# Kernel optimization log

Measured on AMD Instinct MI355X. Metric: run time of the kernel, lower is better.

The kernel has to match this reference:

```python
import jax, jax.numpy as jnp
import numpy as np

D_MODEL = 1024
NUM_HEADS = 16
D_HEAD = D_MODEL // NUM_HEADS
MAX_SEQ_LEN = 2048
THETA = 10000.0
BATCH = 2
SEQ = 2048


def _rope_tables():
    # inv_freq over even dims; emb interleaves each freq twice: [f0,f0,f1,f1,...]
    inv_freq = 1.0 / (THETA ** (jnp.arange(0, D_HEAD, 2, dtype=jnp.float32) / D_HEAD))
    t = jnp.arange(MAX_SEQ_LEN, dtype=jnp.float32)
    freqs = jnp.einsum('i,j->ij', t, inv_freq)  # [S, d_head/2]
    emb = jnp.stack((freqs, freqs), axis=-1).reshape(MAX_SEQ_LEN, D_HEAD)
    return jnp.cos(emb), jnp.sin(emb)


def _rotate_half(x):
    # pairwise interleaved rotation: (x0,x1,x2,x3,...) -> (-x1,x0,-x3,x2,...)
    xr = x.reshape(x.shape[:-1] + (D_HEAD // 2, 2))
    x1, x2 = xr[..., 0], xr[..., 1]
    return jnp.stack((-x2, x1), axis=-1).reshape(x.shape)


def setup_inputs() -> dict:
    key = jax.random.key(0)
    ks = jax.random.split(key, 5)
    std = np.sqrt(2.0 / (D_MODEL + D_MODEL)).astype(np.float32)
    return {
        'in_features': jax.random.normal(ks[0], (BATCH, SEQ, D_MODEL), dtype=jnp.float32),
        'token_positions': jnp.arange(SEQ, dtype=jnp.int64) if jax.config.jax_enable_x64 else jnp.arange(SEQ, dtype=jnp.int32),
        'wq': jax.random.normal(ks[1], (D_MODEL, D_MODEL), dtype=jnp.float32) * std,
        'wk': jax.random.normal(ks[2], (D_MODEL, D_MODEL), dtype=jnp.float32) * std,
        'wv': jax.random.normal(ks[3], (D_MODEL, D_MODEL), dtype=jnp.float32) * std,
        'wo': jax.random.normal(ks[4], (D_MODEL, D_MODEL), dtype=jnp.float32) * std,
    }


def reference(in_features, token_positions, wq, wk, wv, wo):
    b, s, _ = in_features.shape
    cos_tab, sin_tab = _rope_tables()
    cos = cos_tab[token_positions]  # [s, d_head]
    sin = sin_tab[token_positions]

    def split_heads(t):  # [b, s, d_model] -> [b, h, s, d_head]
        return t.reshape(b, s, NUM_HEADS, D_HEAD).transpose(0, 2, 1, 3)

    q = split_heads(jnp.einsum('bsd,ed->bse', in_features, wq))
    k = split_heads(jnp.einsum('bsd,ed->bse', in_features, wk))
    v = split_heads(jnp.einsum('bsd,ed->bse', in_features, wv))

    q = q * cos + _rotate_half(q) * sin
    k = k * cos + _rotate_half(k) * sin

    scale = 1.0 / np.sqrt(D_HEAD).astype(np.float32)
    scores = jnp.einsum('bhqd,bhkd->bhqk', q, k) * scale  # [b,h,s,s]
    causal = jnp.tril(jnp.ones((s, s), dtype=bool))
    scores = jnp.where(causal, scores, -jnp.inf)
    weights = jax.nn.softmax(scores, axis=-1)
    out = jnp.einsum('bhqk,bhkd->bhqd', weights, v)
    out = out.transpose(0, 2, 1, 3).reshape(b, s, D_MODEL)
    return jnp.einsum('bsd,ed->bse', out, wo)
```

## Files before the change

kernel.cpp:

```cpp
#include <hip/hip_runtime.h>


typedef __attribute__((ext_vector_type(8))) short bf16x8;
typedef __attribute__((ext_vector_type(4))) float f32x4;
typedef __attribute__((ext_vector_type(8))) unsigned short u16x8;

__device__ __forceinline__ short f2bf(float f) {
  unsigned u = __float_as_uint(f);
  unsigned r = (u + 0x7fffu + ((u >> 16) & 1u)) >> 16;
  return (short)(r & 0xFFFFu);
}
__device__ __forceinline__ float bf2f(unsigned short b) {
  return __uint_as_float(((unsigned)b) << 16);
}

__device__ __forceinline__ void async16(const void* g, void* l) {
  __builtin_amdgcn_global_load_lds(
      (const __attribute__((address_space(1))) void*)g,
      (__attribute__((address_space(3))) void*)l, 16, 0, 0);
}

__device__ __forceinline__ void cstore(short* C, size_t i, float v) { C[i] = f2bf(v); }
__device__ __forceinline__ void cstore(float* C, size_t i, float v) { C[i] = v; }

__global__ void cast_x_kernel(const float4* __restrict__ src, short* __restrict__ dst) {
  int i = blockIdx.x * 256 + threadIdx.x;
  float4 v = src[i];
  ((short4*)dst)[i] = make_short4(f2bf(v.x), f2bf(v.y), f2bf(v.z), f2bf(v.w));
}

__global__ void cast_w_kernel(const float4* __restrict__ w0, const float4* __restrict__ w1,
                              const float4* __restrict__ w2, const float4* __restrict__ w3,
                              short* __restrict__ dst) {
  int t = blockIdx.x * 256 + threadIdx.x;
  int which = t >> 18;
  int idx = t & 0x3FFFF;
  const float4* s = (which == 0) ? w0 : (which == 1) ? w1 : (which == 2) ? w2 : w3;
  float4 v = s[idx];
  ((short4*)dst)[t] = make_short4(f2bf(v.x), f2bf(v.y), f2bf(v.z), f2bf(v.w));
}

template <typename OUT, int NF>
__device__ __forceinline__ void gemm_core(const short* __restrict__ A, const short* __restrict__ B,
                                          OUT* __restrict__ C, int bm, int bn, int ldc) {
  constexpr int BN = 32 * NF;
  __shared__ __align__(16) short As[2][128 * 32];
  __shared__ __align__(16) short Bs[2][BN * 32];
  const int tid  = threadIdx.x;
  const int lane = tid & 63, wave = tid >> 6;
  const int col  = lane & 15, quad = lane >> 4;
  const int wm = (wave & 1) * 64, wn = (wave >> 1) * (16 * NF);

  f32x4 acc[4][NF];
#pragma unroll
  for (int i = 0; i < 4; i++)
#pragma unroll
    for (int j = 0; j < NF; j++) acc[i][j] = (f32x4){0.f, 0.f, 0.f, 0.f};

  auto stage = [&](int k0, int bu) {
#pragma unroll
    for (int c = tid; c < 512; c += 256) {
      int r = c >> 2, cc = (c & 3) << 3;
      async16(A + (size_t)(bm + r) * 1024 + k0 + cc, As[bu] + c * 8);
    }
#pragma unroll
    for (int c = tid; c < BN * 4; c += 256) {
      int r = c >> 2, cc = (c & 3) << 3;
      async16(B + (size_t)(bn + r) * 1024 + k0 + cc, Bs[bu] + c * 8);
    }
  };

  stage(0, 0);
  for (int it = 0; it < 32; ++it) {
    __syncthreads();
    if (it < 31) stage((it + 1) * 32, (it + 1) & 1);
    const short* as = As[it & 1];
    const short* bs = Bs[it & 1];

    bf16x8 af[4], bfr[NF];
#pragma unroll
    for (int i = 0; i < 4; i++)
      af[i] = *(const bf16x8*)(as + (wm + i * 16 + col) * 32 + quad * 8);
#pragma unroll
    for (int i = 0; i < NF; i++)
      bfr[i] = *(const bf16x8*)(bs + (wn + i * 16 + col) * 32 + quad * 8);
#pragma unroll
    for (int mi = 0; mi < 4; mi++)
#pragma unroll
      for (int ni = 0; ni < NF; ni++)
        acc[mi][ni] = __builtin_amdgcn_mfma_f32_16x16x32_bf16(af[mi], bfr[ni], acc[mi][ni], 0, 0, 0);
  }

#pragma unroll
  for (int mi = 0; mi < 4; mi++) {
#pragma unroll
    for (int r = 0; r < 4; r++) {
      size_t row = (size_t)(bm + wm + mi * 16 + quad * 4 + r);
#pragma unroll
      for (int ni = 0; ni < NF; ni++) {
        int cg = bn + wn + ni * 16 + col;
        cstore(C, row * ldc + cg, acc[mi][ni][r]);
      }
    }
  }
}

__global__ __launch_bounds__(256) void qkv_gemm(const short* __restrict__ Xb,
                                                const short* __restrict__ Wq,
                                                const short* __restrict__ Wk,
                                                const short* __restrict__ Wv,
                                                short* __restrict__ Qo,
                                                short* __restrict__ Ko,
                                                short* __restrict__ Vto) {
  const int z = blockIdx.z;
  if (z == 0)      gemm_core<short, 4>(Xb, Wq, Qo, blockIdx.x * 128, blockIdx.y * 128, 1024);
  else if (z == 1) gemm_core<short, 4>(Xb, Wk, Ko, blockIdx.x * 128, blockIdx.y * 128, 1024);
  else             gemm_core<short, 4>(Wv, Xb, Vto, blockIdx.y * 128, blockIdx.x * 128, 4096);
}

__global__ __launch_bounds__(256) void out_gemm(const short* __restrict__ Ctx,
                                                const short* __restrict__ Wo,
                                                float* __restrict__ C) {
  gemm_core<float, 2>(Ctx, Wo, C, blockIdx.x * 128, blockIdx.y * 64, 1024);
}

__global__ void rope_kernel(short* __restrict__ Q, short* __restrict__ K,
                            const int* __restrict__ pos) {
  int t = blockIdx.x * 256 + threadIdx.x;
  short* P = (t >> 19) ? K : Q;
  int idx  = t & 0x7FFFF;
  int flat = idx << 3;
  int row  = flat >> 10;
  int s    = row & 2047;
  float fp = (float)pos[s];
  int d0   = flat & 63;
  u16x8 v  = *((const u16x8*)P + idx);
#pragma unroll
  for (int j = 0; j < 4; j++) {
    int pr = (d0 >> 1) + j;
    float invf = __expf(-0.28782313662425575f * (float)pr);
    float ang = fp * invf;
    float sn, cs;
    sincosf(ang, &sn, &cs);
    float x0 = bf2f(v[2 * j]);
    float x1 = bf2f(v[2 * j + 1]);
    v[2 * j]     = (unsigned short)f2bf(x0 * cs - x1 * sn);
    v[2 * j + 1] = (unsigned short)f2bf(x1 * cs + x0 * sn);
  }
  *((u16x8*)P + idx) = v;
}

__global__ __launch_bounds__(256) void flash_attn(const short* __restrict__ Q,
                                                  const short* __restrict__ K,
                                                  const short* __restrict__ Vt,
                                                  short* __restrict__ ctx) {
  const int qt = blockIdx.y, bh = blockIdx.x;
  const int b = bh >> 4, h = bh & 15;
  __shared__ __align__(16) short Ks[2][64 * 64];
  __shared__ __align__(16) short Vs[2][64 * 64];
  __shared__ __align__(16) short Ps[4][16 * 64];
  const int tid = threadIdx.x, lane = tid & 63, wave = tid >> 6;
  const int col = lane & 15, quad = lane >> 4;

  const size_t qrow = (size_t)(b * 2048 + qt * 64 + wave * 16 + col);
  bf16x8 qf0 = *(const bf16x8*)(Q + qrow * 1024 + h * 64 + quad * 8);
  bf16x8 qf1 = *(const bf16x8*)(Q + qrow * 1024 + h * 64 + 32 + quad * 8);

  float l_i[4] = {0.f, 0.f, 0.f, 0.f};
  f32x4 o_acc[4];
#pragma unroll
  for (int i = 0; i < 4; i++) o_acc[i] = (f32x4){0.f, 0.f, 0.f, 0.f};

  auto stage = [&](int kt, int bu) {
#pragma unroll
    for (int i = 0; i < 2; i++) {
      int c = i * 256 + tid;
      int r = c >> 3;
      int g = ((c & 7) ^ (r & 7)) << 3;
      async16(K  + (size_t)(b * 2048 + kt * 64 + r) * 1024 + h * 64 + g, Ks[bu] + c * 8);
      async16(Vt + (size_t)(h * 64 + r) * 4096 + b * 2048 + kt * 64 + g, Vs[bu] + c * 8);
    }
  };

  stage(0, 0);
  const int qbase = wave * 16 + quad * 4;
  for (int kt = 0; kt <= qt; ++kt) {
    __syncthreads();
    if (kt < qt) stage(kt + 1, (kt + 1) & 1);
    const short* ks = Ks[kt & 1];
    const short* vs = Vs[kt & 1];

    f32x4 s_acc[4];
#pragma unroll
    for (int nb = 0; nb < 4; nb++) {
      int row = nb * 16 + col;
      bf16x8 k0 = *(const bf16x8*)(ks + (row * 8 + (quad ^ (row & 7))) * 8);
      bf16x8 k1 = *(const bf16x8*)(ks + (row * 8 + ((quad + 4) ^ (row & 7))) * 8);
      f32x4 z = (f32x4){0.f, 0.f, 0.f, 0.f};
      z = __builtin_amdgcn_mfma_f32_16x16x32_bf16(qf0, k0, z, 0, 0, 0);
      z = __builtin_amdgcn_mfma_f32_16x16x32_bf16(qf1, k1, z, 0, 0, 0);
      s_acc[nb] = z;
    }

    const bool diag = (kt == qt);
#pragma unroll
    for (int nb = 0; nb < 4; nb++) {
      int key = nb * 16 + col;
      int chg = key >> 3;
#pragma unroll
      for (int r = 0; r < 4; r++) {
        float p = __expf(s_acc[nb][r] * 0.125f - 12.0f);
        if (diag && key > qbase + r) p = 0.f;
        l_i[r] += p;
        int rowp = quad * 4 + r;
        int slot = rowp * 8 + (chg ^ (rowp & 7));
        Ps[wave][slot * 8 + (key & 7)] = f2bf(p);
      }
    }

    bf16x8 af0 = *(const bf16x8*)(&Ps[wave][(col * 8 + (quad ^ (col & 7))) * 8]);
    bf16x8 af1 = *(const bf16x8*)(&Ps[wave][(col * 8 + ((quad + 4) ^ (col & 7))) * 8]);
#pragma unroll
    for (int nb = 0; nb < 4; nb++) {
      int row = nb * 16 + col;
      bf16x8 v0 = *(const bf16x8*)(vs + (row * 8 + (quad ^ (row & 7))) * 8);
      bf16x8 v1 = *(const bf16x8*)(vs + (row * 8 + ((quad + 4) ^ (row & 7))) * 8);
      o_acc[nb] = __builtin_amdgcn_mfma_f32_16x16x32_bf16(af0, v0, o_acc[nb], 0, 0, 0);
      o_acc[nb] = __builtin_amdgcn_mfma_f32_16x16x32_bf16(af1, v1, o_acc[nb], 0, 0, 0);
    }
  }

#pragma unroll
  for (int r = 0; r < 4; r++) {
#pragma unroll
    for (int off = 1; off < 16; off <<= 1) l_i[r] += __shfl_xor(l_i[r], off);
  }

#pragma unroll
  for (int r = 0; r < 4; r++) {
    float inv = 1.0f / l_i[r];
    size_t row = (size_t)(b * 2048 + qt * 64 + wave * 16 + quad * 4 + r);
#pragma unroll
    for (int nb = 0; nb < 4; nb++)
      ctx[row * 1024 + h * 64 + nb * 16 + col] = f2bf(o_acc[nb][r] * inv);
  }
}

extern "C" void kernel_launch(void* const* d_in, const int* in_sizes, int n_in,
                              void* d_out, int out_size, void* d_ws, size_t ws_size,
                              hipStream_t stream) {
  const float* X  = (const float*)d_in[0];
  const int* pos  = (const int*)d_in[1];
  const float* wq = (const float*)d_in[2];
  const float* wk = (const float*)d_in[3];
  const float* wv = (const float*)d_in[4];
  const float* wo = (const float*)d_in[5];
  float* out = (float*)d_out;

  short* Xb  = (short*)d_ws;
  short* Wqb = Xb + (1 << 22);
  short* Wkb = Wqb + (1 << 20);
  short* Wvb = Wkb + (1 << 20);
  short* Wob = Wvb + (1 << 20);
  short* Qb  = Wob + (1 << 20);
  short* Kb  = Qb + (1 << 22);
  short* Vtb = Kb + (1 << 22);
  short* Ctx = Vtb + (1 << 22);

  cast_x_kernel<<<4096, 256, 0, stream>>>((const float4*)X, Xb);
  cast_w_kernel<<<4096, 256, 0, stream>>>((const float4*)wq, (const float4*)wk,
                                          (const float4*)wv, (const float4*)wo, Wqb);
  qkv_gemm<<<dim3(32, 8, 3), 256, 0, stream>>>(Xb, Wqb, Wkb, Wvb, Qb, Kb, Vtb);
  rope_kernel<<<4096, 256, 0, stream>>>(Qb, Kb, pos);
  flash_attn<<<dim3(32, 32), 256, 0, stream>>>(Qb, Kb, Vtb, Ctx);
  out_gemm<<<dim3(32, 16), 256, 0, stream>>>(Ctx, Wob, out);
}
```

Before: 195.3 us.

## Fuse RoPE into QKV GEMM, merge casts, rebalance and streamline flash attention

Merges the two cast kernels into one launch and applies RoPE inside the Q/K GEMM epilogue, using a lane shuffle for the pair rotation, so the separate rope pass over Q and K is dropped. In flash attention it interleaves query-tile order so long and short causal blocks are mixed, and swaps the QK^T MFMA operands so each lane holds one query row. That lets the row sum live in a single scalar and the P tile be written as packed bf16 pairs. The diagonal tile is split out of the loop and exp2 with folded constants is used. The fixed-offset softmax with no running max and the round-half-up packing keep the same numeric risk profile as before.

```diff
diff --git a/kernel.cpp b/kernel.cpp
--- a/kernel.cpp
+++ b/kernel.cpp
@@ -3,15 +3,16 @@
 
 typedef __attribute__((ext_vector_type(8))) short bf16x8;
 typedef __attribute__((ext_vector_type(4))) float f32x4;
-typedef __attribute__((ext_vector_type(8))) unsigned short u16x8;
 
 __device__ __forceinline__ short f2bf(float f) {
   unsigned u = __float_as_uint(f);
   unsigned r = (u + 0x7fffu + ((u >> 16) & 1u)) >> 16;
   return (short)(r & 0xFFFFu);
 }
-__device__ __forceinline__ float bf2f(unsigned short b) {
-  return __uint_as_float(((unsigned)b) << 16);
+
+__device__ __forceinline__ unsigned pk2(float a, float b) {
+  return __builtin_amdgcn_perm(__float_as_uint(b) + 0x8000u,
+                               __float_as_uint(a) + 0x8000u, 0x07060302u);
 }
 
 __device__ __forceinline__ void async16(const void* g, void* l) {
@@ -23,26 +24,29 @@
 __device__ __forceinline__ void cstore(short* C, size_t i, float v) { C[i] = f2bf(v); }
 __device__ __forceinline__ void cstore(float* C, size_t i, float v) { C[i] = v; }
 
-__global__ void cast_x_kernel(const float4* __restrict__ src, short* __restrict__ dst) {
-  int i = blockIdx.x * 256 + threadIdx.x;
-  float4 v = src[i];
-  ((short4*)dst)[i] = make_short4(f2bf(v.x), f2bf(v.y), f2bf(v.z), f2bf(v.w));
-}
-
-__global__ void cast_w_kernel(const float4* __restrict__ w0, const float4* __restrict__ w1,
-                              const float4* __restrict__ w2, const float4* __restrict__ w3,
-                              short* __restrict__ dst) {
+__global__ void cast_all(const float4* __restrict__ X,
+                         const float4* __restrict__ w0, const float4* __restrict__ w1,
+                         const float4* __restrict__ w2, const float4* __restrict__ w3,
+                         short* __restrict__ Xb, short* __restrict__ Wb) {
   int t = blockIdx.x * 256 + threadIdx.x;
-  int which = t >> 18;
-  int idx = t & 0x3FFFF;
-  const float4* s = (which == 0) ? w0 : (which == 1) ? w1 : (which == 2) ? w2 : w3;
-  float4 v = s[idx];
-  ((short4*)dst)[t] = make_short4(f2bf(v.x), f2bf(v.y), f2bf(v.z), f2bf(v.w));
-}
-
-template <typename OUT, int NF>
+  const float4* s;
+  short4* d;
+  if (t < (1 << 20)) {
+    s = X + t; d = (short4*)Xb + t;
+  } else {
+    int u = t - (1 << 20);
+    int which = u >> 18;
+    s = ((which == 0) ? w0 : (which == 1) ? w1 : (which == 2) ? w2 : w3) + (u & 0x3FFFF);
+    d = (short4*)Wb + u;
+  }
+  float4 v = *s;
+  *d = make_short4(f2bf(v.x), f2bf(v.y), f2bf(v.z), f2bf(v.w));
+}
+
+template <typename OUT, int NF, bool ROPE>
 __device__ __forceinline__ void gemm_core(const short* __restrict__ A, const short* __restrict__ B,
-                                          OUT* __restrict__ C, int bm, int bn, int ldc) {
+                                          OUT* __restrict__ C, int bm, int bn, int ldc,
+                                          const int* __restrict__ pos) {
   constexpr int BN = 32 * NF;
   __shared__ __align__(16) short As[2][128 * 32];
   __shared__ __align__(16) short Bs[2][BN * 32];
@@ -91,6 +95,33 @@
         acc[mi][ni] = __builtin_amdgcn_mfma_f32_16x16x32_bf16(af[mi], bfr[ni], acc[mi][ni], 0, 0, 0);
   }
 
+  if (ROPE) {
+    float invf[NF];
+#pragma unroll
+    for (int ni = 0; ni < NF; ni++) {
+      int pr = ((bn + wn + ni * 16 + col) & 63) >> 1;
+      invf[ni] = exp2f(-0.4152410118609203f * (float)pr);
+    }
+    const float sgn = (col & 1) ? 1.f : -1.f;
+#pragma unroll
+    for (int mi = 0; mi < 4; mi++) {
+#pragma unroll
+      for (int r = 0; r < 4; r++) {
+        int row = bm + wm + mi * 16 + quad * 4 + r;
+        float fp = (float)pos[row & 2047];
+#pragma unroll
+        for (int ni = 0; ni < NF; ni++) {
+          float ang = fp * invf[ni];
+          float sn, cs;
+          sincosf(ang, &sn, &cs);
+          float x  = acc[mi][ni][r];
+          float px = __shfl_xor(x, 1);
+          acc[mi][ni][r] = fmaf(x, cs, sgn * px * sn);
+        }
+      }
+    }
+  }
+
 #pragma unroll
   for (int mi = 0; mi < 4; mi++) {
 #pragma unroll
@@ -111,50 +142,27 @@
                                                 const short* __restrict__ Wv,
                                                 short* __restrict__ Qo,
                                                 short* __restrict__ Ko,
-                                                short* __restrict__ Vto) {
+                                                short* __restrict__ Vto,
+                                                const int* __restrict__ pos) {
   const int z = blockIdx.z;
-  if (z == 0)      gemm_core<short, 4>(Xb, Wq, Qo, blockIdx.x * 128, blockIdx.y * 128, 1024);
-  else if (z == 1) gemm_core<short, 4>(Xb, Wk, Ko, blockIdx.x * 128, blockIdx.y * 128, 1024);
-  else             gemm_core<short, 4>(Wv, Xb, Vto, blockIdx.y * 128, blockIdx.x * 128, 4096);
+  if (z == 0)      gemm_core<short, 4, true >(Xb, Wq, Qo, blockIdx.x * 128, blockIdx.y * 128, 1024, pos);
+  else if (z == 1) gemm_core<short, 4, true >(Xb, Wk, Ko, blockIdx.x * 128, blockIdx.y * 128, 1024, pos);
+  else             gemm_core<short, 4, false>(Wv, Xb, Vto, blockIdx.y * 128, blockIdx.x * 128, 4096, pos);
 }
 
 __global__ __launch_bounds__(256) void out_gemm(const short* __restrict__ Ctx,
                                                 const short* __restrict__ Wo,
                                                 float* __restrict__ C) {
-  gemm_core<float, 2>(Ctx, Wo, C, blockIdx.x * 128, blockIdx.y * 64, 1024);
-}
-
-__global__ void rope_kernel(short* __restrict__ Q, short* __restrict__ K,
-                            const int* __restrict__ pos) {
-  int t = blockIdx.x * 256 + threadIdx.x;
-  short* P = (t >> 19) ? K : Q;
-  int idx  = t & 0x7FFFF;
-  int flat = idx << 3;
-  int row  = flat >> 10;
-  int s    = row & 2047;
-  float fp = (float)pos[s];
-  int d0   = flat & 63;
-  u16x8 v  = *((const u16x8*)P + idx);
-#pragma unroll
-  for (int j = 0; j < 4; j++) {
-    int pr = (d0 >> 1) + j;
-    float invf = __expf(-0.28782313662425575f * (float)pr);
-    float ang = fp * invf;
-    float sn, cs;
-    sincosf(ang, &sn, &cs);
-    float x0 = bf2f(v[2 * j]);
-    float x1 = bf2f(v[2 * j + 1]);
-    v[2 * j]     = (unsigned short)f2bf(x0 * cs - x1 * sn);
-    v[2 * j + 1] = (unsigned short)f2bf(x1 * cs + x0 * sn);
-  }
-  *((u16x8*)P + idx) = v;
+  gemm_core<float, 2, false>(Ctx, Wo, C, blockIdx.x * 128, blockIdx.y * 64, 1024, nullptr);
 }
 
 __global__ __launch_bounds__(256) void flash_attn(const short* __restrict__ Q,
                                                   const short* __restrict__ K,
                                                   const short* __restrict__ Vt,
                                                   short* __restrict__ ctx) {
-  const int qt = blockIdx.y, bh = blockIdx.x;
+  const int y = blockIdx.y, a = y & 7, kk = y >> 3;
+  const int qt = (kk == 0) ? 2 * a : (kk == 1) ? 31 - 2 * a : (kk == 2) ? 2 * a + 1 : 30 - 2 * a;
+  const int bh = blockIdx.x;
   const int b = bh >> 4, h = bh & 15;
   __shared__ __align__(16) short Ks[2][64 * 64];
   __shared__ __align__(16) short Vs[2][64 * 64];
@@ -166,7 +174,7 @@
   bf16x8 qf0 = *(const bf16x8*)(Q + qrow * 1024 + h * 64 + quad * 8);
   bf16x8 qf1 = *(const bf16x8*)(Q + qrow * 1024 + h * 64 + 32 + quad * 8);
 
-  float l_i[4] = {0.f, 0.f, 0.f, 0.f};
+  float l_i = 0.f;
   f32x4 o_acc[4];
 #pragma unroll
   for (int i = 0; i < 4; i++) o_acc[i] = (f32x4){0.f, 0.f, 0.f, 0.f};
@@ -182,14 +190,21 @@
     }
   };
 
-  stage(0, 0);
-  const int qbase = wave * 16 + quad * 4;
-  for (int kt = 0; kt <= qt; ++kt) {
-    __syncthreads();
-    if (kt < qt) stage(kt + 1, (kt + 1) & 1);
+  int pswr[4], psrd0, psrd1;
+#pragma unroll
+  for (int nb = 0; nb < 4; nb++) {
+    int c8 = nb * 2 + (quad >> 1);
+    pswr[nb] = col * 64 + ((c8 ^ (col & 7)) << 3) + (quad & 1) * 4;
+  }
+  psrd0 = col * 64 + ((quad ^ (col & 7)) << 3);
+  psrd1 = col * 64 + (((quad + 4) ^ (col & 7)) << 3);
+
+  const float C1 = 0.18033688011112042f;
+  const float C2 = 17.31234049066756f;
+
+  auto tile = [&](int kt, bool diag) {
     const short* ks = Ks[kt & 1];
     const short* vs = Vs[kt & 1];
-
     f32x4 s_acc[4];
 #pragma unroll
     for (int nb = 0; nb < 4; nb++) {
@@ -197,29 +212,23 @@
       bf16x8 k0 = *(const bf16x8*)(ks + (row * 8 + (quad ^ (row & 7))) * 8);
       bf16x8 k1 = *(const bf16x8*)(ks + (row * 8 + ((quad + 4) ^ (row & 7))) * 8);
       f32x4 z = (f32x4){0.f, 0.f, 0.f, 0.f};
-      z = __builtin_amdgcn_mfma_f32_16x16x32_bf16(qf0, k0, z, 0, 0, 0);
-      z = __builtin_amdgcn_mfma_f32_16x16x32_bf16(qf1, k1, z, 0, 0, 0);
+      z = __builtin_amdgcn_mfma_f32_16x16x32_bf16(k0, qf0, z, 0, 0, 0);
+      z = __builtin_amdgcn_mfma_f32_16x16x32_bf16(k1, qf1, z, 0, 0, 0);
       s_acc[nb] = z;
     }
-
-    const bool diag = (kt == qt);
 #pragma unroll
     for (int nb = 0; nb < 4; nb++) {
-      int key = nb * 16 + col;
-      int chg = key >> 3;
+      float p[4];
 #pragma unroll
       for (int r = 0; r < 4; r++) {
-        float p = __expf(s_acc[nb][r] * 0.125f - 12.0f);
-        if (diag && key > qbase + r) p = 0.f;
-        l_i[r] += p;
-        int rowp = quad * 4 + r;
-        int slot = rowp * 8 + (chg ^ (rowp & 7));
-        Ps[wave][slot * 8 + (key & 7)] = f2bf(p);
+        p[r] = exp2f(s_acc[nb][r] * C1 - C2);
+        if (diag && (nb * 16 + quad * 4 + r) > (wave * 16 + col)) p[r] = 0.f;
+        l_i += p[r];
       }
-    }
-
-    bf16x8 af0 = *(const bf16x8*)(&Ps[wave][(col * 8 + (quad ^ (col & 7))) * 8]);
-    bf16x8 af1 = *(const bf16x8*)(&Ps[wave][(col * 8 + ((quad + 4) ^ (col & 7))) * 8]);
+      *(uint2*)(&Ps[wave][pswr[nb]]) = make_uint2(pk2(p[0], p[1]), pk2(p[2], p[3]));
+    }
+    bf16x8 af0 = *(const bf16x8*)(&Ps[wave][psrd0]);
+    bf16x8 af1 = *(const bf16x8*)(&Ps[wave][psrd1]);
 #pragma unroll
     for (int nb = 0; nb < 4; nb++) {
       int row = nb * 16 + col;
@@ -228,17 +237,24 @@
       o_acc[nb] = __builtin_amdgcn_mfma_f32_16x16x32_bf16(af0, v0, o_acc[nb], 0, 0, 0);
       o_acc[nb] = __builtin_amdgcn_mfma_f32_16x16x32_bf16(af1, v1, o_acc[nb], 0, 0, 0);
     }
-  }
+  };
+
+  stage(0, 0);
+  for (int kt = 0; kt < qt; ++kt) {
+    __syncthreads();
+    stage(kt + 1, (kt + 1) & 1);
+    tile(kt, false);
+  }
+  __syncthreads();
+  tile(qt, true);
+
+  l_i += __shfl_xor(l_i, 16);
+  l_i += __shfl_xor(l_i, 32);
+  float invl = 1.0f / l_i;
 
 #pragma unroll
   for (int r = 0; r < 4; r++) {
-#pragma unroll
-    for (int off = 1; off < 16; off <<= 1) l_i[r] += __shfl_xor(l_i[r], off);
-  }
-
-#pragma unroll
-  for (int r = 0; r < 4; r++) {
-    float inv = 1.0f / l_i[r];
+    float inv = __shfl(invl, quad * 4 + r);
     size_t row = (size_t)(b * 2048 + qt * 64 + wave * 16 + quad * 4 + r);
 #pragma unroll
     for (int nb = 0; nb < 4; nb++)
@@ -267,11 +283,9 @@
   short* Vtb = Kb + (1 << 22);
   short* Ctx = Vtb + (1 << 22);
 
-  cast_x_kernel<<<4096, 256, 0, stream>>>((const float4*)X, Xb);
-  cast_w_kernel<<<4096, 256, 0, stream>>>((const float4*)wq, (const float4*)wk,
-                                          (const float4*)wv, (const float4*)wo, Wqb);
-  qkv_gemm<<<dim3(32, 8, 3), 256, 0, stream>>>(Xb, Wqb, Wkb, Wvb, Qb, Kb, Vtb);
-  rope_kernel<<<4096, 256, 0, stream>>>(Qb, Kb, pos);
+  cast_all<<<8192, 256, 0, stream>>>((const float4*)X, (const float4*)wq, (const float4*)wk,
+                                     (const float4*)wv, (const float4*)wo, Xb, Wqb);
+  qkv_gemm<<<dim3(32, 8, 3), 256, 0, stream>>>(Xb, Wqb, Wkb, Wvb, Qb, Kb, Vtb, pos);
   flash_attn<<<dim3(32, 32), 256, 0, stream>>>(Qb, Kb, Vtb, Ctx);
   out_gemm<<<dim3(32, 16), 256, 0, stream>>>(Ctx, Wob, out);
 }
```

Measured after the change: 434.5 us. 122% more time.
